# Performance work log

Hardware: AMD Instinct MI355X
Metric: run time of the kernel (lower is better)

The kernel has to match this reference:

```python
import jax, jax.numpy as jnp
import numpy as np

# Model dims (match init_kwargs)
E = 16            # real experts
Z = 16            # zero experts (identity)
TOP_K = 4
H = 1024          # hidden_size
I = 512           # intermediate_size per expert
T = 4096          # tokens
ROUTED_SCALING = 1.0


def setup_inputs() -> dict:
    key = jax.random.key(0)
    ks = jax.random.split(key, 6)
    s_h = 1.0 / np.sqrt(H)
    s_i = 1.0 / np.sqrt(I)
    return {
        "hidden_states": jax.random.normal(ks[0], (T, H), jnp.float32),
        # router over E + Z total slots (real experts + zero experts)
        "router_weight": jax.random.normal(ks[1], (E + Z, H), jnp.float32) * s_h,
        "e_score_bias": jax.random.normal(ks[2], (E + Z,), jnp.float32) * 0.01,
        # SwiGLU expert weights
        "w_gate": jax.random.normal(ks[3], (E, H, I), jnp.float32) * s_h,
        "w_up": jax.random.normal(ks[4], (E, H, I), jnp.float32) * s_h,
        "w_down": jax.random.normal(ks[5], (E, I, H), jnp.float32) * s_i,
    }


def reference(hidden_states, router_weight, e_score_bias, w_gate, w_up, w_down):
    x = hidden_states  # [T, H]
    # --- Router (float32, router_dtype == 'float32') ---
    logits = jnp.einsum("th,eh->te", x.astype(jnp.float32), router_weight)  # [T, E+Z]
    scores = jax.nn.softmax(logits, axis=-1)
    # top-k selected on bias-corrected scores; weights taken from raw scores,
    # renormalize=False
    _, topk_ids = jax.lax.top_k(scores + e_score_bias[None, :], TOP_K)  # [T, k]
    topk_w = jnp.take_along_axis(scores, topk_ids, axis=-1)             # [T, k]
    # --- Dispatch/combine weights over all E+Z slots ---
    onehot = jax.nn.one_hot(topk_ids, E + Z, dtype=jnp.float32)  # [T, k, E+Z]
    combine = jnp.einsum("tk,tks->ts", topk_w, onehot)           # [T, E+Z]
    cw_real = combine[:, :E].astype(x.dtype)      # [T, E] routed-expert weights
    zero_w = combine[:, E:].sum(-1).astype(x.dtype)  # [T] identity weight sum
    # --- Grouped-expert SwiGLU (dense dispatch reference) ---
    g = jnp.einsum("th,ehi->eti", x, w_gate)   # [E, T, I]
    u = jnp.einsum("th,ehi->eti", x, w_up)     # [E, T, I]
    act = jax.nn.silu(g) * u
    eout = jnp.einsum("eti,eih->eth", act, w_down)  # [E, T, H]
    routed = jnp.einsum("eth,te->th", eout, cw_real)  # [T, H]
    # zero experts: identity contribution (zero_expert_type == 'identity')
    out = routed * ROUTED_SCALING + zero_w[:, None] * x
    return out
```

## Files before the change

kernel.cpp:

```cpp
#include <hip/hip_runtime.h>
#include <stdint.h>

#define T_TOK 4096
#define Hd    1024
#define Id    512
#define NE    16
#define NSLOT 32
#define TOPK  4
#define ECAP  1024
#define MAXT  (NE * (ECAP/128))

typedef __bf16 bf16x8 __attribute__((ext_vector_type(8)));
typedef float  floatx4 __attribute__((ext_vector_type(4)));

#define WAIT_VM(n) asm volatile("s_waitcnt vmcnt(" #n ")" ::: "memory")

static __device__ __forceinline__ void wg_barrier(){
  asm volatile("" ::: "memory");
  __builtin_amdgcn_s_barrier();
  asm volatile("" ::: "memory");
}

static __device__ __forceinline__ unsigned short f2bf(float f){
  unsigned int u = __float_as_uint(f);
  u = u + 0x7fffu + ((u >> 16) & 1u);
  return (unsigned short)(u >> 16);
}

static __device__ __forceinline__ void load_lds16(const void* g, void* l){
  __builtin_amdgcn_global_load_lds((const __attribute__((address_space(1))) void*)g,
                                   (__attribute__((address_space(3))) void*)l, 16, 0, 0);
}

__global__ __launch_bounds__(256) void prep_kernel(
    const float* __restrict__ wg, const float* __restrict__ wu,
    const float* __restrict__ wd, const float* __restrict__ x,
    const float* __restrict__ rw,
    unsigned short* __restrict__ wgb, unsigned short* __restrict__ wub,
    unsigned short* __restrict__ wdb, unsigned short* __restrict__ xb,
    float* __restrict__ logits, int* __restrict__ cursors){
  __shared__ float shbuf[2*64*65];
  const int bid = blockIdx.x;
  const int tid = threadIdx.x;
  if (bid < 640){
    const float* src; unsigned short* dst; int R, C, e, r0;
    if (bid < 256)      { src = wg; dst = wgb; R = Hd; C = Id; e = bid >> 4;        r0 = (bid & 15) * 64; }
    else if (bid < 512) { src = wu; dst = wub; R = Hd; C = Id; e = (bid - 256) >> 4; r0 = (bid & 15) * 64; }
    else                { src = wd; dst = wdb; R = Id; C = Hd; e = (bid - 512) >> 3; r0 = ((bid - 512) & 7) * 64; }
    const int J = C >> 6;
    const float* s = src + (size_t)e * R * C + (size_t)r0 * C;
    unsigned short* d = dst + (size_t)e * R * C + r0;
    const int lr = tid >> 4;
    const int lc = (tid & 15) * 4;
    float* b0 = shbuf;
    float* b1 = shbuf + 64*65;
    float4 v[4];
    #pragma unroll
    for (int p = 0; p < 4; ++p)
      v[p] = *(const float4*)(s + (size_t)(p*16 + lr)*C + lc);
    #pragma unroll
    for (int p = 0; p < 4; ++p){
      float* row = b0 + (p*16 + lr)*65 + lc;
      row[0] = v[p].x; row[1] = v[p].y; row[2] = v[p].z; row[3] = v[p].w;
    }
    __syncthreads();
    for (int j = 0; j < J; ++j){
      float* cur = (j & 1) ? b1 : b0;
      float* nxt = (j & 1) ? b0 : b1;
      if (j + 1 < J){
        const int c0n = (j + 1) * 64;
        #pragma unroll
        for (int p = 0; p < 4; ++p)
          v[p] = *(const float4*)(s + (size_t)(p*16 + lr)*C + c0n + lc);
      }
      const int c0 = j * 64;
      #pragma unroll
      for (int p = 0; p < 4; ++p){
        int c = p*16 + lr;
        ushort4 o;
        o.x = f2bf(cur[(lc+0)*65 + c]); o.y = f2bf(cur[(lc+1)*65 + c]);
        o.z = f2bf(cur[(lc+2)*65 + c]); o.w = f2bf(cur[(lc+3)*65 + c]);
        *(ushort4*)(d + (size_t)(c0 + c)*R + lc) = o;
      }
      if (j + 1 < J){
        #pragma unroll
        for (int p = 0; p < 4; ++p){
          float* row = nxt + (p*16 + lr)*65 + lc;
          row[0] = v[p].x; row[1] = v[p].y; row[2] = v[p].z; row[3] = v[p].w;
        }
      }
      __syncthreads();
    }
  } else if (bid < 1664){
    const int ib = (bid - 640) * 1024;
    #pragma unroll
    for (int p = 0; p < 4; ++p){
      int i = ib + p*256 + tid;
      float4 v = ((const float4*)x)[i];
      ushort4 o;
      o.x = f2bf(v.x); o.y = f2bf(v.y); o.z = f2bf(v.z); o.w = f2bf(v.w);
      ((ushort4*)xb)[i] = o;
    }
  } else {
    const int lb = bid - 1664;
    if (lb == 0 && tid < NE) cursors[tid] = 0;
    float* srw = shbuf;
    const int t  = lb * 32 + (tid >> 3);
    const int s0 = tid & 7;
    float4 acc = {0.f, 0.f, 0.f, 0.f};
    for (int c = 0; c < 4; ++c){
      const int kc = c * 256;
      __syncthreads();
      #pragma unroll
      for (int p = 0; p < 8; ++p){
        int idx = tid + p*256;
        int s = idx >> 6;
        int col = (idx & 63) << 2;
        *(float4*)&srw[s*260 + col] = *(const float4*)(rw + (size_t)s*Hd + kc + col);
      }
      __syncthreads();
      for (int k = 0; k < 256; k += 4){
        float4 xv = *(const float4*)(x + (size_t)t*Hd + kc + k);
        float4 r0 = *(const float4*)&srw[(s0+ 0)*260 + k];
        float4 r1 = *(const float4*)&srw[(s0+ 8)*260 + k];
        float4 r2 = *(const float4*)&srw[(s0+16)*260 + k];
        float4 r3 = *(const float4*)&srw[(s0+24)*260 + k];
        acc.x += xv.x*r0.x + xv.y*r0.y + xv.z*r0.z + xv.w*r0.w;
        acc.y += xv.x*r1.x + xv.y*r1.y + xv.z*r1.z + xv.w*r1.w;
        acc.z += xv.x*r2.x + xv.y*r2.y + xv.z*r2.z + xv.w*r2.w;
        acc.w += xv.x*r3.x + xv.y*r3.y + xv.z*r3.z + xv.w*r3.w;
      }
    }
    logits[(size_t)t*NSLOT + s0     ] = acc.x;
    logits[(size_t)t*NSLOT + s0 +  8] = acc.y;
    logits[(size_t)t*NSLOT + s0 + 16] = acc.z;
    logits[(size_t)t*NSLOT + s0 + 24] = acc.w;
  }
}

__global__ __launch_bounds__(256) void topk_kernel(
    const float* __restrict__ logits, const float* __restrict__ bias,
    const float* __restrict__ x,
    int* __restrict__ cursors, int* __restrict__ rowmap, float* __restrict__ roww,
    float* __restrict__ out){
  __shared__ float szw[8];
  const int tid = threadIdx.x;
  if (tid < 8){
    const int t = blockIdx.x * 8 + tid;
    float sc[32], bsc[32];
    #pragma unroll
    for (int i = 0; i < 32; i += 4){
      float4 v = *(const float4*)(logits + (size_t)t*NSLOT + i);
      sc[i] = v.x; sc[i+1] = v.y; sc[i+2] = v.z; sc[i+3] = v.w;
    }
    float mx = sc[0];
    #pragma unroll
    for (int i = 1; i < 32; ++i) mx = fmaxf(mx, sc[i]);
    float sum = 0.f;
    #pragma unroll
    for (int i = 0; i < 32; ++i){ sc[i] = __expf(sc[i]-mx); sum += sc[i]; }
    float inv = 1.f / sum;
    #pragma unroll
    for (int i = 0; i < 32; ++i){ sc[i] *= inv; bsc[i] = sc[i] + bias[i]; }
    unsigned int chosen = 0;
    float zw = 0.f;
    #pragma unroll
    for (int k = 0; k < TOPK; ++k){
      float bv = -1e30f, bw = 0.f; int best = 0;
      #pragma unroll
      for (int i = 0; i < 32; ++i){
        float v = ((chosen >> i) & 1u) ? -1e30f : bsc[i];
        if (v > bv){ bv = v; best = i; bw = sc[i]; }
      }
      chosen |= (1u << best);
      if (best < NE){
        int pos = atomicAdd(&cursors[best], 1);
        rowmap[best*ECAP + pos] = t;
        roww[best*ECAP + pos]   = bw;
      } else zw += bw;
    }
    szw[tid] = zw;
  }
  __syncthreads();
  const int lane = tid & 63, wid = tid >> 6;
  const size_t base = (size_t)blockIdx.x * 8 * Hd;
  #pragma unroll
  for (int r0 = 0; r0 < 8; r0 += 4){
    int r = r0 + wid;
    float s = szw[r];
    const float4* xs = (const float4*)(x + base + (size_t)r*Hd);
    float4* os = (float4*)(out + base + (size_t)r*Hd);
    #pragma unroll
    for (int q = 0; q < 4; ++q){
      float4 v = xs[lane + q*64];
      float4 o; o.x = v.x*s; o.y = v.y*s; o.z = v.z*s; o.w = v.w*s;
      os[lane + q*64] = o;
    }
  }
}

static __device__ __forceinline__ bool tile_map(const int* __restrict__ counts, int tile,
                                                int& e, int& off, int& ne, int& m0){
  int cumT = 0; e = -1; ne = 0; m0 = 0;
  #pragma unroll
  for (int ee = 0; ee < NE; ++ee){
    int c = counts[ee];
    int nt = (c + 127) >> 7;
    bool here = (e < 0) && (tile < cumT + nt);
    if (here){ e = ee; ne = c; m0 = (tile - cumT) * 128; }
    cumT += nt;
  }
  off = (e >= 0) ? e * ECAP : 0;
  return e >= 0;
}

__global__ __launch_bounds__(256, 2) void gateup_kernel(
    const unsigned short* __restrict__ xb,
    const unsigned short* __restrict__ wgb,
    const unsigned short* __restrict__ wub,
    const int* __restrict__ counts,
    const int* __restrict__ rowmap,
    const float* __restrict__ roww,
    unsigned short* __restrict__ act){
  const int b = blockIdx.x;
  int e, off, ne, m0;
  if (!tile_map(counts, b >> 2, e, off, ne, m0)) return;
  const int n0 = (b & 3) * 128;

  __shared__ unsigned short sA [2][128*32];
  __shared__ unsigned short sBg[2][128*32];
  __shared__ unsigned short sBu[2][128*32];
  __shared__ int sT[128];

  const int tid  = threadIdx.x;
  const int lane = tid & 63;
  const int wid  = tid >> 6;

  if (tid < 128){
    int r = m0 + tid;
    sT[tid] = rowmap[off + ((r < ne) ? r : 0)];
  }
  __syncthreads();

  const int r_in = lane >> 2;
  const int seg  = lane & 3;
  const int rt0  = wid*32 + r_in;
  const int rt1  = rt0 + 16;
  const size_t wbase = (size_t)e * Id * Hd;

  const unsigned short* pA0 = xb + (size_t)sT[rt0]*Hd + seg*8;
  const unsigned short* pA1 = xb + (size_t)sT[rt1]*Hd + seg*8;
  const unsigned short* pG0 = wgb + wbase + (size_t)(n0+rt0)*Hd + seg*8;
  const unsigned short* pG1 = wgb + wbase + (size_t)(n0+rt1)*Hd + seg*8;
  const unsigned short* pU0 = wub + wbase + (size_t)(n0+rt0)*Hd + seg*8;
  const unsigned short* pU1 = wub + wbase + (size_t)(n0+rt1)*Hd + seg*8;
  const int dA0 = wid*1024;
  const int dA1 = wid*1024 + 512;

  floatx4 accg[4][4], accu[4][4];
  #pragma unroll
  for (int i = 0; i < 4; ++i)
    #pragma unroll
    for (int j = 0; j < 4; ++j){
      floatx4 z = {0.f,0.f,0.f,0.f};
      accg[i][j] = z; accu[i][j] = z;
    }

  const int wm = (wid & 1) * 64;
  const int wn = (wid >> 1) * 64;
  const int fm = lane & 15;
  const int fq = lane >> 4;

  load_lds16(pA0, &sA[0][dA0]);  load_lds16(pA1, &sA[0][dA1]);
  load_lds16(pG0, &sBg[0][dA0]); load_lds16(pG1, &sBg[0][dA1]);
  load_lds16(pU0, &sBu[0][dA0]); load_lds16(pU1, &sBu[0][dA1]);

  #pragma unroll 2
  for (int kit = 0; kit < 32; ++kit){
    const int cur = kit & 1;
    if (kit < 31){
      const int nk = (kit+1)*32;
      const int nb = 1 - cur;
      load_lds16(pA0 + nk, &sA[nb][dA0]);  load_lds16(pA1 + nk, &sA[nb][dA1]);
      load_lds16(pG0 + nk, &sBg[nb][dA0]); load_lds16(pG1 + nk, &sBg[nb][dA1]);
      load_lds16(pU0 + nk, &sBu[nb][dA0]); load_lds16(pU1 + nk, &sBu[nb][dA1]);
      WAIT_VM(6);
    } else {
      WAIT_VM(0);
    }
    wg_barrier();
    bf16x8 av[4], bgv[4], buv[4];
    #pragma unroll
    for (int i = 0; i < 4; ++i)
      av[i] = *(const bf16x8*)(&sA[cur][(wm + i*16 + fm)*32 + fq*8]);
    #pragma unroll
    for (int j = 0; j < 4; ++j){
      bgv[j] = *(const bf16x8*)(&sBg[cur][(wn + j*16 + fm)*32 + fq*8]);
      buv[j] = *(const bf16x8*)(&sBu[cur][(wn + j*16 + fm)*32 + fq*8]);
    }
    #pragma unroll
    for (int i = 0; i < 4; ++i)
      #pragma unroll
      for (int j = 0; j < 4; ++j){
        accg[i][j] = __builtin_amdgcn_mfma_f32_16x16x32_bf16(av[i], bgv[j], accg[i][j], 0, 0, 0);
        accu[i][j] = __builtin_amdgcn_mfma_f32_16x16x32_bf16(av[i], buv[j], accu[i][j], 0, 0, 0);
      }
    wg_barrier();
  }

  #pragma unroll
  for (int i = 0; i < 4; ++i){
    #pragma unroll
    for (int r = 0; r < 4; ++r){
      int row = wm + i*16 + fq*4 + r;
      if (m0 + row < ne){
        float w = roww[off + m0 + row];
        size_t rb = (size_t)(off + m0 + row) * Id + n0;
        #pragma unroll
        for (int j = 0; j < 4; ++j){
          float g = accg[i][j][r];
          float u = accu[i][j][r];
          float a = (g / (1.f + __expf(-g))) * u * w;
          act[rb + wn + j*16 + fm] = f2bf(a);
        }
      }
    }
  }
}

__global__ __launch_bounds__(256, 4) void down_kernel(
    const unsigned short* __restrict__ act,
    const unsigned short* __restrict__ wdb,
    const int* __restrict__ counts,
    const int* __restrict__ rowmap,
    float* __restrict__ out){
  const int b = blockIdx.x;
  int e, off, ne, m0;
  if (!tile_map(counts, b >> 3, e, off, ne, m0)) return;
  const int n0 = (b & 7) * 128;

  __shared__ unsigned short sA[2][128*32];
  __shared__ unsigned short sB[2][128*32];
  __shared__ int sT[128];

  const int tid  = threadIdx.x;
  const int lane = tid & 63;
  const int wid  = tid >> 6;
  if (tid < 128){
    int r = m0 + tid;
    sT[tid] = (r < ne) ? rowmap[off + r] : 0;
  }

  const int r_in = lane >> 2, seg = lane & 3;
  const int rt0 = wid*32 + r_in;
  const int rt1 = rt0 + 16;
  const int gr0 = off + ((m0 + rt0 < ne) ? (m0 + rt0) : 0);
  const int gr1 = off + ((m0 + rt1 < ne) ? (m0 + rt1) : 0);
  const size_t wbase = (size_t)e * Hd * Id;
  const unsigned short* pA0 = act + (size_t)gr0*Id + seg*8;
  const unsigned short* pA1 = act + (size_t)gr1*Id + seg*8;
  const unsigned short* pB0 = wdb + wbase + (size_t)(n0+rt0)*Id + seg*8;
  const unsigned short* pB1 = wdb + wbase + (size_t)(n0+rt1)*Id + seg*8;
  const int dA0 = wid*1024, dA1 = wid*1024 + 512;

  floatx4 acc[4][4];
  #pragma unroll
  for (int i = 0; i < 4; ++i)
    #pragma unroll
    for (int j = 0; j < 4; ++j){ floatx4 z = {0.f,0.f,0.f,0.f}; acc[i][j] = z; }

  const int wm = (wid & 1) * 64, wn = (wid >> 1) * 64;
  const int fm = lane & 15, fq = lane >> 4;

  load_lds16(pA0, &sA[0][dA0]); load_lds16(pA1, &sA[0][dA1]);
  load_lds16(pB0, &sB[0][dA0]); load_lds16(pB1, &sB[0][dA1]);

  #pragma unroll 2
  for (int kit = 0; kit < 16; ++kit){
    const int cur = kit & 1;
    if (kit < 15){
      const int nk = (kit+1)*32;
      const int nb = 1 - cur;
      load_lds16(pA0 + nk, &sA[nb][dA0]); load_lds16(pA1 + nk, &sA[nb][dA1]);
      load_lds16(pB0 + nk, &sB[nb][dA0]); load_lds16(pB1 + nk, &sB[nb][dA1]);
      WAIT_VM(4);
    } else {
      WAIT_VM(0);
    }
    wg_barrier();
    bf16x8 av[4], bv[4];
    #pragma unroll
    for (int i = 0; i < 4; ++i) av[i] = *(const bf16x8*)(&sA[cur][(wm + i*16 + fm)*32 + fq*8]);
    #pragma unroll
    for (int j = 0; j < 4; ++j) bv[j] = *(const bf16x8*)(&sB[cur][(wn + j*16 + fm)*32 + fq*8]);
    #pragma unroll
    for (int i = 0; i < 4; ++i)
      #pragma unroll
      for (int j = 0; j < 4; ++j)
        acc[i][j] = __builtin_amdgcn_mfma_f32_16x16x32_bf16(av[i], bv[j], acc[i][j], 0, 0, 0);
    wg_barrier();
  }

  #pragma unroll
  for (int i = 0; i < 4; ++i){
    #pragma unroll
    for (int r = 0; r < 4; ++r){
      int row = wm + i*16 + fq*4 + r;
      if (m0 + row < ne){
        int t = sT[row];
        #pragma unroll
        for (int j = 0; j < 4; ++j)
          atomicAdd(&out[(size_t)t*Hd + n0 + wn + j*16 + fm], acc[i][j][r]);
      }
    }
  }
}

extern "C" void kernel_launch(void* const* d_in, const int* in_sizes, int n_in,
                              void* d_out, int out_size, void* d_ws, size_t ws_size,
                              hipStream_t stream){
  (void)in_sizes; (void)n_in; (void)out_size; (void)ws_size;
  const float* x    = (const float*)d_in[0];
  const float* rw   = (const float*)d_in[1];
  const float* bias = (const float*)d_in[2];
  const float* wg   = (const float*)d_in[3];
  const float* wu   = (const float*)d_in[4];
  const float* wd   = (const float*)d_in[5];
  float* out = (float*)d_out;

  char* ws = (char*)d_ws;
  const size_t WSZ = (size_t)NE * Id * Hd * 2;
  unsigned short* wgb = (unsigned short*)(ws);
  unsigned short* wub = (unsigned short*)(ws + WSZ);
  unsigned short* wdb = (unsigned short*)(ws + 2*WSZ);
  unsigned short* xb  = (unsigned short*)(ws + 3*WSZ);
  unsigned short* act = (unsigned short*)(ws + 3*WSZ + (size_t)T_TOK*Hd*2);
  char* misc = ws + 3*WSZ + (size_t)T_TOK*Hd*2 + (size_t)NE*ECAP*Id*2;

  const size_t LOGB = (size_t)T_TOK * NSLOT * 4;
  float* logits  = (float*)misc;
  int*   cursors = (int*)(misc + LOGB);
  char* p2 = misc + LOGB + 256;
  int*   rowmap = (int*)p2;                     p2 += (size_t)NE*ECAP*4;
  float* roww   = (float*)p2;

  prep_kernel<<<1792, 256, 0, stream>>>(wg, wu, wd, x, rw,
                                        wgb, wub, wdb, xb, logits, cursors);
  topk_kernel<<<T_TOK/8, 256, 0, stream>>>(logits, bias, x, cursors, rowmap, roww, out);
  gateup_kernel<<<MAXT*4, 256, 0, stream>>>(xb, wgb, wub, cursors, rowmap, roww, act);
  down_kernel<<<MAXT*8, 256, 0, stream>>>(act, wdb, cursors, rowmap, out);
}
```

Measured before the change: 304.4 us.

## Fuse fp32-to-bf16 weight conversion into the expert GEMM B-tile loads

Drops the separate prep pass that transposed and converted all expert weights to bf16. The gate/up and down GEMMs now read fp32 weights directly into registers, truncate pairs to bf16 with a byte permute, and write them into padded LDS tiles, with a register prefetch two iterations ahead. This removes a full read and write of the weight tensors per call, at the cost of reading fp32 weights once per token tile and spending VALU time on packing. Weight rounding changes from round-to-nearest to truncation, and the barrier is replaced with explicit lgkmcnt waits.

```diff
diff --git a/kernel.cpp b/kernel.cpp
--- a/kernel.cpp
+++ b/kernel.cpp
@@ -14,11 +14,13 @@
 typedef float  floatx4 __attribute__((ext_vector_type(4)));
 
 #define WAIT_VM(n) asm volatile("s_waitcnt vmcnt(" #n ")" ::: "memory")
-
+#define CFENCE()   asm volatile("" ::: "memory")
+
+static __device__ __forceinline__ void barrier_lgkm(){
+  asm volatile("s_waitcnt lgkmcnt(0)\ns_barrier" ::: "memory");
+}
 static __device__ __forceinline__ void wg_barrier(){
-  asm volatile("" ::: "memory");
-  __builtin_amdgcn_s_barrier();
-  asm volatile("" ::: "memory");
+  asm volatile("s_barrier" ::: "memory");
 }
 
 static __device__ __forceinline__ unsigned short f2bf(float f){
@@ -32,69 +34,39 @@
                                    (__attribute__((address_space(3))) void*)l, 16, 0, 0);
 }
 
+struct B8 { float4 a0, a1, b0, b1; };
+
+static __device__ __forceinline__ B8 loadB(const float* p, int S){
+  B8 r;
+  r.a0 = *(const float4*)(p);
+  r.a1 = *(const float4*)(p + 4);
+  r.b0 = *(const float4*)(p + S);
+  r.b1 = *(const float4*)(p + S + 4);
+  return r;
+}
+
+static __device__ __forceinline__ void packB(const B8& r, uint32_t* dst, int ng8, int kq){
+  dst[(ng8+0)*20 + kq] = __builtin_amdgcn_perm(__float_as_uint(r.b0.x), __float_as_uint(r.a0.x), 0x07060302u);
+  dst[(ng8+1)*20 + kq] = __builtin_amdgcn_perm(__float_as_uint(r.b0.y), __float_as_uint(r.a0.y), 0x07060302u);
+  dst[(ng8+2)*20 + kq] = __builtin_amdgcn_perm(__float_as_uint(r.b0.z), __float_as_uint(r.a0.z), 0x07060302u);
+  dst[(ng8+3)*20 + kq] = __builtin_amdgcn_perm(__float_as_uint(r.b0.w), __float_as_uint(r.a0.w), 0x07060302u);
+  dst[(ng8+4)*20 + kq] = __builtin_amdgcn_perm(__float_as_uint(r.b1.x), __float_as_uint(r.a1.x), 0x07060302u);
+  dst[(ng8+5)*20 + kq] = __builtin_amdgcn_perm(__float_as_uint(r.b1.y), __float_as_uint(r.a1.y), 0x07060302u);
+  dst[(ng8+6)*20 + kq] = __builtin_amdgcn_perm(__float_as_uint(r.b1.z), __float_as_uint(r.a1.z), 0x07060302u);
+  dst[(ng8+7)*20 + kq] = __builtin_amdgcn_perm(__float_as_uint(r.b1.w), __float_as_uint(r.a1.w), 0x07060302u);
+}
+
 __global__ __launch_bounds__(256) void prep_kernel(
-    const float* __restrict__ wg, const float* __restrict__ wu,
-    const float* __restrict__ wd, const float* __restrict__ x,
-    const float* __restrict__ rw,
-    unsigned short* __restrict__ wgb, unsigned short* __restrict__ wub,
-    unsigned short* __restrict__ wdb, unsigned short* __restrict__ xb,
-    float* __restrict__ logits, int* __restrict__ cursors){
-  __shared__ float shbuf[2*64*65];
+    const float* __restrict__ x, const float* __restrict__ rw,
+    unsigned short* __restrict__ xb, float* __restrict__ logits,
+    int* __restrict__ cursors){
+  __shared__ float srw[NSLOT*260];
   const int bid = blockIdx.x;
   const int tid = threadIdx.x;
-  if (bid < 640){
-    const float* src; unsigned short* dst; int R, C, e, r0;
-    if (bid < 256)      { src = wg; dst = wgb; R = Hd; C = Id; e = bid >> 4;        r0 = (bid & 15) * 64; }
-    else if (bid < 512) { src = wu; dst = wub; R = Hd; C = Id; e = (bid - 256) >> 4; r0 = (bid & 15) * 64; }
-    else                { src = wd; dst = wdb; R = Id; C = Hd; e = (bid - 512) >> 3; r0 = ((bid - 512) & 7) * 64; }
-    const int J = C >> 6;
-    const float* s = src + (size_t)e * R * C + (size_t)r0 * C;
-    unsigned short* d = dst + (size_t)e * R * C + r0;
-    const int lr = tid >> 4;
-    const int lc = (tid & 15) * 4;
-    float* b0 = shbuf;
-    float* b1 = shbuf + 64*65;
-    float4 v[4];
-    #pragma unroll
-    for (int p = 0; p < 4; ++p)
-      v[p] = *(const float4*)(s + (size_t)(p*16 + lr)*C + lc);
-    #pragma unroll
-    for (int p = 0; p < 4; ++p){
-      float* row = b0 + (p*16 + lr)*65 + lc;
-      row[0] = v[p].x; row[1] = v[p].y; row[2] = v[p].z; row[3] = v[p].w;
-    }
-    __syncthreads();
-    for (int j = 0; j < J; ++j){
-      float* cur = (j & 1) ? b1 : b0;
-      float* nxt = (j & 1) ? b0 : b1;
-      if (j + 1 < J){
-        const int c0n = (j + 1) * 64;
-        #pragma unroll
-        for (int p = 0; p < 4; ++p)
-          v[p] = *(const float4*)(s + (size_t)(p*16 + lr)*C + c0n + lc);
-      }
-      const int c0 = j * 64;
-      #pragma unroll
-      for (int p = 0; p < 4; ++p){
-        int c = p*16 + lr;
-        ushort4 o;
-        o.x = f2bf(cur[(lc+0)*65 + c]); o.y = f2bf(cur[(lc+1)*65 + c]);
-        o.z = f2bf(cur[(lc+2)*65 + c]); o.w = f2bf(cur[(lc+3)*65 + c]);
-        *(ushort4*)(d + (size_t)(c0 + c)*R + lc) = o;
-      }
-      if (j + 1 < J){
-        #pragma unroll
-        for (int p = 0; p < 4; ++p){
-          float* row = nxt + (p*16 + lr)*65 + lc;
-          row[0] = v[p].x; row[1] = v[p].y; row[2] = v[p].z; row[3] = v[p].w;
-        }
-      }
-      __syncthreads();
-    }
-  } else if (bid < 1664){
-    const int ib = (bid - 640) * 1024;
-    #pragma unroll
-    for (int p = 0; p < 4; ++p){
+  if (bid < 256){
+    const int ib = bid * 4096;
+    #pragma unroll
+    for (int p = 0; p < 16; ++p){
       int i = ib + p*256 + tid;
       float4 v = ((const float4*)x)[i];
       ushort4 o;
@@ -102,9 +74,8 @@
       ((ushort4*)xb)[i] = o;
     }
   } else {
-    const int lb = bid - 1664;
+    const int lb = bid - 256;
     if (lb == 0 && tid < NE) cursors[tid] = 0;
-    float* srw = shbuf;
     const int t  = lb * 32 + (tid >> 3);
     const int s0 = tid & 7;
     float4 acc = {0.f, 0.f, 0.f, 0.f};
@@ -216,46 +187,34 @@
 
 __global__ __launch_bounds__(256, 2) void gateup_kernel(
     const unsigned short* __restrict__ xb,
-    const unsigned short* __restrict__ wgb,
-    const unsigned short* __restrict__ wub,
-    const int* __restrict__ counts,
-    const int* __restrict__ rowmap,
-    const float* __restrict__ roww,
-    unsigned short* __restrict__ act){
+    const float* __restrict__ wg, const float* __restrict__ wu,
+    const int* __restrict__ counts, const int* __restrict__ rowmap,
+    const float* __restrict__ roww, unsigned short* __restrict__ act){
   const int b = blockIdx.x;
   int e, off, ne, m0;
   if (!tile_map(counts, b >> 2, e, off, ne, m0)) return;
   const int n0 = (b & 3) * 128;
 
   __shared__ unsigned short sA [2][128*32];
-  __shared__ unsigned short sBg[2][128*32];
-  __shared__ unsigned short sBu[2][128*32];
+  __shared__ unsigned short sBg[2][128*40];
+  __shared__ unsigned short sBu[2][128*40];
   __shared__ int sT[128];
 
-  const int tid  = threadIdx.x;
-  const int lane = tid & 63;
-  const int wid  = tid >> 6;
-
-  if (tid < 128){
-    int r = m0 + tid;
-    sT[tid] = rowmap[off + ((r < ne) ? r : 0)];
-  }
+  const int tid = threadIdx.x, lane = tid & 63, wid = tid >> 6;
+  if (tid < 128){ int r = m0 + tid; sT[tid] = rowmap[off + ((r < ne) ? r : 0)]; }
   __syncthreads();
 
-  const int r_in = lane >> 2;
-  const int seg  = lane & 3;
-  const int rt0  = wid*32 + r_in;
-  const int rt1  = rt0 + 16;
-  const size_t wbase = (size_t)e * Id * Hd;
-
+  const int r_in = lane >> 2, seg = lane & 3;
+  const int rt0 = wid*32 + r_in, rt1 = rt0 + 16;
   const unsigned short* pA0 = xb + (size_t)sT[rt0]*Hd + seg*8;
   const unsigned short* pA1 = xb + (size_t)sT[rt1]*Hd + seg*8;
-  const unsigned short* pG0 = wgb + wbase + (size_t)(n0+rt0)*Hd + seg*8;
-  const unsigned short* pG1 = wgb + wbase + (size_t)(n0+rt1)*Hd + seg*8;
-  const unsigned short* pU0 = wub + wbase + (size_t)(n0+rt0)*Hd + seg*8;
-  const unsigned short* pU1 = wub + wbase + (size_t)(n0+rt1)*Hd + seg*8;
-  const int dA0 = wid*1024;
-  const int dA1 = wid*1024 + 512;
+  const int dA0 = wid*1024, dA1 = wid*1024 + 512;
+
+  const size_t wbase = (size_t)e * Hd * Id;
+  const int ng8 = (tid >> 4) * 8;
+  const int kq  = tid & 15;
+  const float* pG = wg + wbase + (size_t)(kq*2)*Id + n0 + ng8;
+  const float* pU = wu + wbase + (size_t)(kq*2)*Id + n0 + ng8;
 
   floatx4 accg[4][4], accu[4][4];
   #pragma unroll
@@ -265,38 +224,44 @@
       floatx4 z = {0.f,0.f,0.f,0.f};
       accg[i][j] = z; accu[i][j] = z;
     }
-
-  const int wm = (wid & 1) * 64;
-  const int wn = (wid >> 1) * 64;
-  const int fm = lane & 15;
-  const int fq = lane >> 4;
-
-  load_lds16(pA0, &sA[0][dA0]);  load_lds16(pA1, &sA[0][dA1]);
-  load_lds16(pG0, &sBg[0][dA0]); load_lds16(pG1, &sBg[0][dA1]);
-  load_lds16(pU0, &sBu[0][dA0]); load_lds16(pU1, &sBu[0][dA1]);
-
-  #pragma unroll 2
+  const int wm = (wid & 1) * 64, wn = (wid >> 1) * 64;
+  const int fm = lane & 15, fq = lane >> 4;
+
+  B8 rg = loadB(pG, Id);
+  B8 ru = loadB(pU, Id);
+  load_lds16(pA0, &sA[0][dA0]); load_lds16(pA1, &sA[0][dA1]);
+  CFENCE();
+  packB(rg, (uint32_t*)&sBg[0][0], ng8, kq);
+  packB(ru, (uint32_t*)&sBu[0][0], ng8, kq);
+  CFENCE();
+  rg = loadB(pG + (size_t)32*Id, Id);
+  ru = loadB(pU + (size_t)32*Id, Id);
+
   for (int kit = 0; kit < 32; ++kit){
     const int cur = kit & 1;
     if (kit < 31){
-      const int nk = (kit+1)*32;
       const int nb = 1 - cur;
-      load_lds16(pA0 + nk, &sA[nb][dA0]);  load_lds16(pA1 + nk, &sA[nb][dA1]);
-      load_lds16(pG0 + nk, &sBg[nb][dA0]); load_lds16(pG1 + nk, &sBg[nb][dA1]);
-      load_lds16(pU0 + nk, &sBu[nb][dA0]); load_lds16(pU1 + nk, &sBu[nb][dA1]);
-      WAIT_VM(6);
-    } else {
-      WAIT_VM(0);
-    }
-    wg_barrier();
+      const int nk = (kit + 1) * 32;
+      load_lds16(pA0 + nk, &sA[nb][dA0]);
+      load_lds16(pA1 + nk, &sA[nb][dA1]);
+      CFENCE();
+      packB(rg, (uint32_t*)&sBg[nb][0], ng8, kq);
+      packB(ru, (uint32_t*)&sBu[nb][0], ng8, kq);
+      CFENCE();
+      const size_t k2 = (size_t)((kit < 30) ? (kit + 2) : 31) * 32;
+      rg = loadB(pG + k2*Id, Id);
+      ru = loadB(pU + k2*Id, Id);
+      WAIT_VM(8);
+    }
+    barrier_lgkm();
     bf16x8 av[4], bgv[4], buv[4];
     #pragma unroll
     for (int i = 0; i < 4; ++i)
       av[i] = *(const bf16x8*)(&sA[cur][(wm + i*16 + fm)*32 + fq*8]);
     #pragma unroll
     for (int j = 0; j < 4; ++j){
-      bgv[j] = *(const bf16x8*)(&sBg[cur][(wn + j*16 + fm)*32 + fq*8]);
-      buv[j] = *(const bf16x8*)(&sBu[cur][(wn + j*16 + fm)*32 + fq*8]);
+      bgv[j] = *(const bf16x8*)(&sBg[cur][(wn + j*16 + fm)*40 + fq*8]);
+      buv[j] = *(const bf16x8*)(&sBu[cur][(wn + j*16 + fm)*40 + fq*8]);
     }
     #pragma unroll
     for (int i = 0; i < 4; ++i)
@@ -330,9 +295,8 @@
 
 __global__ __launch_bounds__(256, 4) void down_kernel(
     const unsigned short* __restrict__ act,
-    const unsigned short* __restrict__ wdb,
-    const int* __restrict__ counts,
-    const int* __restrict__ rowmap,
+    const float* __restrict__ wd,
+    const int* __restrict__ counts, const int* __restrict__ rowmap,
     float* __restrict__ out){
   const int b = blockIdx.x;
   int e, off, ne, m0;
@@ -340,59 +304,61 @@
   const int n0 = (b & 7) * 128;
 
   __shared__ unsigned short sA[2][128*32];
-  __shared__ unsigned short sB[2][128*32];
+  __shared__ unsigned short sB[2][128*40];
   __shared__ int sT[128];
 
-  const int tid  = threadIdx.x;
-  const int lane = tid & 63;
-  const int wid  = tid >> 6;
-  if (tid < 128){
-    int r = m0 + tid;
-    sT[tid] = (r < ne) ? rowmap[off + r] : 0;
-  }
+  const int tid = threadIdx.x, lane = tid & 63, wid = tid >> 6;
+  if (tid < 128){ int r = m0 + tid; sT[tid] = (r < ne) ? rowmap[off + r] : 0; }
+  __syncthreads();
 
   const int r_in = lane >> 2, seg = lane & 3;
-  const int rt0 = wid*32 + r_in;
-  const int rt1 = rt0 + 16;
+  const int rt0 = wid*32 + r_in, rt1 = rt0 + 16;
   const int gr0 = off + ((m0 + rt0 < ne) ? (m0 + rt0) : 0);
   const int gr1 = off + ((m0 + rt1 < ne) ? (m0 + rt1) : 0);
-  const size_t wbase = (size_t)e * Hd * Id;
   const unsigned short* pA0 = act + (size_t)gr0*Id + seg*8;
   const unsigned short* pA1 = act + (size_t)gr1*Id + seg*8;
-  const unsigned short* pB0 = wdb + wbase + (size_t)(n0+rt0)*Id + seg*8;
-  const unsigned short* pB1 = wdb + wbase + (size_t)(n0+rt1)*Id + seg*8;
   const int dA0 = wid*1024, dA1 = wid*1024 + 512;
 
+  const size_t wbase = (size_t)e * Id * Hd;
+  const int ng8 = (tid >> 4) * 8;
+  const int kq  = tid & 15;
+  const float* pB = wd + wbase + (size_t)(kq*2)*Hd + n0 + ng8;
+
   floatx4 acc[4][4];
   #pragma unroll
   for (int i = 0; i < 4; ++i)
     #pragma unroll
     for (int j = 0; j < 4; ++j){ floatx4 z = {0.f,0.f,0.f,0.f}; acc[i][j] = z; }
-
   const int wm = (wid & 1) * 64, wn = (wid >> 1) * 64;
   const int fm = lane & 15, fq = lane >> 4;
 
+  B8 rb = loadB(pB, Hd);
   load_lds16(pA0, &sA[0][dA0]); load_lds16(pA1, &sA[0][dA1]);
-  load_lds16(pB0, &sB[0][dA0]); load_lds16(pB1, &sB[0][dA1]);
-
-  #pragma unroll 2
+  CFENCE();
+  packB(rb, (uint32_t*)&sB[0][0], ng8, kq);
+  CFENCE();
+  rb = loadB(pB + (size_t)32*Hd, Hd);
+
   for (int kit = 0; kit < 16; ++kit){
     const int cur = kit & 1;
     if (kit < 15){
-      const int nk = (kit+1)*32;
       const int nb = 1 - cur;
-      load_lds16(pA0 + nk, &sA[nb][dA0]); load_lds16(pA1 + nk, &sA[nb][dA1]);
-      load_lds16(pB0 + nk, &sB[nb][dA0]); load_lds16(pB1 + nk, &sB[nb][dA1]);
+      const int nk = (kit + 1) * 32;
+      load_lds16(pA0 + nk, &sA[nb][dA0]);
+      load_lds16(pA1 + nk, &sA[nb][dA1]);
+      CFENCE();
+      packB(rb, (uint32_t*)&sB[nb][0], ng8, kq);
+      CFENCE();
+      const size_t k2 = (size_t)((kit < 14) ? (kit + 2) : 15) * 32;
+      rb = loadB(pB + k2*Hd, Hd);
       WAIT_VM(4);
-    } else {
-      WAIT_VM(0);
-    }
-    wg_barrier();
+    }
+    barrier_lgkm();
     bf16x8 av[4], bv[4];
     #pragma unroll
     for (int i = 0; i < 4; ++i) av[i] = *(const bf16x8*)(&sA[cur][(wm + i*16 + fm)*32 + fq*8]);
     #pragma unroll
-    for (int j = 0; j < 4; ++j) bv[j] = *(const bf16x8*)(&sB[cur][(wn + j*16 + fm)*32 + fq*8]);
+    for (int j = 0; j < 4; ++j) bv[j] = *(const bf16x8*)(&sB[cur][(wn + j*16 + fm)*40 + fq*8]);
     #pragma unroll
     for (int i = 0; i < 4; ++i)
       #pragma unroll
@@ -429,13 +395,9 @@
   float* out = (float*)d_out;
 
   char* ws = (char*)d_ws;
-  const size_t WSZ = (size_t)NE * Id * Hd * 2;
-  unsigned short* wgb = (unsigned short*)(ws);
-  unsigned short* wub = (unsigned short*)(ws + WSZ);
-  unsigned short* wdb = (unsigned short*)(ws + 2*WSZ);
-  unsigned short* xb  = (unsigned short*)(ws + 3*WSZ);
-  unsigned short* act = (unsigned short*)(ws + 3*WSZ + (size_t)T_TOK*Hd*2);
-  char* misc = ws + 3*WSZ + (size_t)T_TOK*Hd*2 + (size_t)NE*ECAP*Id*2;
+  unsigned short* xb  = (unsigned short*)ws;
+  unsigned short* act = (unsigned short*)(ws + (size_t)T_TOK*Hd*2);
+  char* misc = ws + (size_t)T_TOK*Hd*2 + (size_t)NE*ECAP*Id*2;
 
   const size_t LOGB = (size_t)T_TOK * NSLOT * 4;
   float* logits  = (float*)misc;
@@ -444,9 +406,8 @@
   int*   rowmap = (int*)p2;                     p2 += (size_t)NE*ECAP*4;
   float* roww   = (float*)p2;
 
-  prep_kernel<<<1792, 256, 0, stream>>>(wg, wu, wd, x, rw,
-                                        wgb, wub, wdb, xb, logits, cursors);
+  prep_kernel<<<384, 256, 0, stream>>>(x, rw, xb, logits, cursors);
   topk_kernel<<<T_TOK/8, 256, 0, stream>>>(logits, bias, x, cursors, rowmap, roww, out);
-  gateup_kernel<<<MAXT*4, 256, 0, stream>>>(xb, wgb, wub, cursors, rowmap, roww, act);
-  down_kernel<<<MAXT*8, 256, 0, stream>>>(act, wdb, cursors, rowmap, out);
-}
+  gateup_kernel<<<MAXT*4, 256, 0, stream>>>(xb, wg, wu, cursors, rowmap, roww, act);
+  down_kernel<<<MAXT*8, 256, 0, stream>>>(act, wd, cursors, rowmap, out);
+}
```

Result: slower. 312.6 us (+2.7%).

## Restructure prep kernel: register-only weight transpose, reordered router and x-convert blocks

Applied to the files above, without the earlier changes.

Rewrites the weight fp32→bf16 transpose so each block handles one 64x64 tile held entirely in registers. Each thread loads four rows of float4 and packs the bf16 pairs with a byte permute, which truncates instead of rounding. This removes the LDS staging, the barriers and the serial per-row loop, and spreads the work across many more blocks. The router-logit blocks now come first with 16 threads per token, and the x conversion uses fewer, larger blocks. In exchange, the transposed stores are 8-byte strided writes rather than coalesced ones, and the truncating conversion changes numerics slightly.

```diff
diff --git a/kernel.cpp b/kernel.cpp
--- a/kernel.cpp
+++ b/kernel.cpp
@@ -27,6 +27,10 @@
   return (unsigned short)(u >> 16);
 }
 
+static __device__ __forceinline__ uint32_t bfpack(uint32_t hi_src, uint32_t lo_src){
+  return __builtin_amdgcn_perm(hi_src, lo_src, 0x07060302u);
+}
+
 static __device__ __forceinline__ void load_lds16(const void* g, void* l){
   __builtin_amdgcn_global_load_lds((const __attribute__((address_space(1))) void*)g,
                                    (__attribute__((address_space(3))) void*)l, 16, 0, 0);
@@ -39,75 +43,14 @@
     unsigned short* __restrict__ wgb, unsigned short* __restrict__ wub,
     unsigned short* __restrict__ wdb, unsigned short* __restrict__ xb,
     float* __restrict__ logits, int* __restrict__ cursors){
-  __shared__ float shbuf[2*64*65];
   const int bid = blockIdx.x;
   const int tid = threadIdx.x;
-  if (bid < 640){
-    const float* src; unsigned short* dst; int R, C, e, r0;
-    if (bid < 256)      { src = wg; dst = wgb; R = Hd; C = Id; e = bid >> 4;        r0 = (bid & 15) * 64; }
-    else if (bid < 512) { src = wu; dst = wub; R = Hd; C = Id; e = (bid - 256) >> 4; r0 = (bid & 15) * 64; }
-    else                { src = wd; dst = wdb; R = Id; C = Hd; e = (bid - 512) >> 3; r0 = ((bid - 512) & 7) * 64; }
-    const int J = C >> 6;
-    const float* s = src + (size_t)e * R * C + (size_t)r0 * C;
-    unsigned short* d = dst + (size_t)e * R * C + r0;
-    const int lr = tid >> 4;
-    const int lc = (tid & 15) * 4;
-    float* b0 = shbuf;
-    float* b1 = shbuf + 64*65;
-    float4 v[4];
-    #pragma unroll
-    for (int p = 0; p < 4; ++p)
-      v[p] = *(const float4*)(s + (size_t)(p*16 + lr)*C + lc);
-    #pragma unroll
-    for (int p = 0; p < 4; ++p){
-      float* row = b0 + (p*16 + lr)*65 + lc;
-      row[0] = v[p].x; row[1] = v[p].y; row[2] = v[p].z; row[3] = v[p].w;
-    }
-    __syncthreads();
-    for (int j = 0; j < J; ++j){
-      float* cur = (j & 1) ? b1 : b0;
-      float* nxt = (j & 1) ? b0 : b1;
-      if (j + 1 < J){
-        const int c0n = (j + 1) * 64;
-        #pragma unroll
-        for (int p = 0; p < 4; ++p)
-          v[p] = *(const float4*)(s + (size_t)(p*16 + lr)*C + c0n + lc);
-      }
-      const int c0 = j * 64;
-      #pragma unroll
-      for (int p = 0; p < 4; ++p){
-        int c = p*16 + lr;
-        ushort4 o;
-        o.x = f2bf(cur[(lc+0)*65 + c]); o.y = f2bf(cur[(lc+1)*65 + c]);
-        o.z = f2bf(cur[(lc+2)*65 + c]); o.w = f2bf(cur[(lc+3)*65 + c]);
-        *(ushort4*)(d + (size_t)(c0 + c)*R + lc) = o;
-      }
-      if (j + 1 < J){
-        #pragma unroll
-        for (int p = 0; p < 4; ++p){
-          float* row = nxt + (p*16 + lr)*65 + lc;
-          row[0] = v[p].x; row[1] = v[p].y; row[2] = v[p].z; row[3] = v[p].w;
-        }
-      }
-      __syncthreads();
-    }
-  } else if (bid < 1664){
-    const int ib = (bid - 640) * 1024;
-    #pragma unroll
-    for (int p = 0; p < 4; ++p){
-      int i = ib + p*256 + tid;
-      float4 v = ((const float4*)x)[i];
-      ushort4 o;
-      o.x = f2bf(v.x); o.y = f2bf(v.y); o.z = f2bf(v.z); o.w = f2bf(v.w);
-      ((ushort4*)xb)[i] = o;
-    }
-  } else {
-    const int lb = bid - 1664;
-    if (lb == 0 && tid < NE) cursors[tid] = 0;
-    float* srw = shbuf;
-    const int t  = lb * 32 + (tid >> 3);
-    const int s0 = tid & 7;
-    float4 acc = {0.f, 0.f, 0.f, 0.f};
+  if (bid < 256){
+    __shared__ float srw[NSLOT*260];
+    if (bid == 0 && tid < NE) cursors[tid] = 0;
+    const int t  = bid * 16 + (tid >> 4);
+    const int s0 = tid & 15;
+    float accx = 0.f, accy = 0.f;
     for (int c = 0; c < 4; ++c){
       const int kc = c * 256;
       __syncthreads();
@@ -121,20 +64,54 @@
       __syncthreads();
       for (int k = 0; k < 256; k += 4){
         float4 xv = *(const float4*)(x + (size_t)t*Hd + kc + k);
-        float4 r0 = *(const float4*)&srw[(s0+ 0)*260 + k];
-        float4 r1 = *(const float4*)&srw[(s0+ 8)*260 + k];
-        float4 r2 = *(const float4*)&srw[(s0+16)*260 + k];
-        float4 r3 = *(const float4*)&srw[(s0+24)*260 + k];
-        acc.x += xv.x*r0.x + xv.y*r0.y + xv.z*r0.z + xv.w*r0.w;
-        acc.y += xv.x*r1.x + xv.y*r1.y + xv.z*r1.z + xv.w*r1.w;
-        acc.z += xv.x*r2.x + xv.y*r2.y + xv.z*r2.z + xv.w*r2.w;
-        acc.w += xv.x*r3.x + xv.y*r3.y + xv.z*r3.z + xv.w*r3.w;
-      }
-    }
-    logits[(size_t)t*NSLOT + s0     ] = acc.x;
-    logits[(size_t)t*NSLOT + s0 +  8] = acc.y;
-    logits[(size_t)t*NSLOT + s0 + 16] = acc.z;
-    logits[(size_t)t*NSLOT + s0 + 24] = acc.w;
+        float4 r0 = *(const float4*)&srw[(s0     )*260 + k];
+        float4 r1 = *(const float4*)&srw[(s0 + 16)*260 + k];
+        accx += xv.x*r0.x + xv.y*r0.y + xv.z*r0.z + xv.w*r0.w;
+        accy += xv.x*r1.x + xv.y*r1.y + xv.z*r1.z + xv.w*r1.w;
+      }
+    }
+    logits[(size_t)t*NSLOT + s0     ] = accx;
+    logits[(size_t)t*NSLOT + s0 + 16] = accy;
+  } else if (bid < 512){
+    const int ib = (bid - 256) * 4096;
+    #pragma unroll
+    for (int p = 0; p < 16; ++p){
+      int i = ib + p*256 + tid;
+      float4 v = ((const float4*)x)[i];
+      ushort4 o;
+      o.x = f2bf(v.x); o.y = f2bf(v.y); o.z = f2bf(v.z); o.w = f2bf(v.w);
+      ((ushort4*)xb)[i] = o;
+    }
+  } else {
+    const int tb = bid - 512;
+    const float* src; unsigned short* dst; int R, C, rt, ct;
+    const int arr = tb >> 11;
+    const int rem = tb & 2047;
+    const int e  = rem >> 7;
+    const int t2 = rem & 127;
+    if (arr == 0)      { src = wg; dst = wgb; R = Hd; C = Id; rt = t2 >> 3; ct = t2 & 7;  }
+    else if (arr == 1) { src = wu; dst = wub; R = Hd; C = Id; rt = t2 >> 3; ct = t2 & 7;  }
+    else               { src = wd; dst = wdb; R = Id; C = Hd; rt = t2 >> 4; ct = t2 & 15; }
+    const int r0 = rt * 64, c0 = ct * 64;
+    const float* s = src + (size_t)e * R * C;
+    unsigned short* d = dst + (size_t)e * R * C;
+    const int r_idx = tid >> 4;
+    const int c_idx = tid & 15;
+    const int rr = r0 + r_idx * 4;
+    const int cc = c0 + c_idx * 4;
+    uint4 u0 = *(const uint4*)(s + (size_t)(rr + 0)*C + cc);
+    uint4 u1 = *(const uint4*)(s + (size_t)(rr + 1)*C + cc);
+    uint4 u2 = *(const uint4*)(s + (size_t)(rr + 2)*C + cc);
+    uint4 u3 = *(const uint4*)(s + (size_t)(rr + 3)*C + cc);
+    uint2 o;
+    o.x = bfpack(u1.x, u0.x); o.y = bfpack(u3.x, u2.x);
+    *(uint2*)(d + (size_t)(cc + 0)*R + rr) = o;
+    o.x = bfpack(u1.y, u0.y); o.y = bfpack(u3.y, u2.y);
+    *(uint2*)(d + (size_t)(cc + 1)*R + rr) = o;
+    o.x = bfpack(u1.z, u0.z); o.y = bfpack(u3.z, u2.z);
+    *(uint2*)(d + (size_t)(cc + 2)*R + rr) = o;
+    o.x = bfpack(u1.w, u0.w); o.y = bfpack(u3.w, u2.w);
+    *(uint2*)(d + (size_t)(cc + 3)*R + rr) = o;
   }
 }
 
@@ -232,20 +209,12 @@
   __shared__ unsigned short sBu[2][128*32];
   __shared__ int sT[128];
 
-  const int tid  = threadIdx.x;
-  const int lane = tid & 63;
-  const int wid  = tid >> 6;
-
-  if (tid < 128){
-    int r = m0 + tid;
-    sT[tid] = rowmap[off + ((r < ne) ? r : 0)];
-  }
+  const int tid = threadIdx.x, lane = tid & 63, wid = tid >> 6;
+  if (tid < 128){ int r = m0 + tid; sT[tid] = rowmap[off + ((r < ne) ? r : 0)]; }
   __syncthreads();
 
-  const int r_in = lane >> 2;
-  const int seg  = lane & 3;
-  const int rt0  = wid*32 + r_in;
-  const int rt1  = rt0 + 16;
+  const int r_in = lane >> 2, seg = lane & 3;
+  const int rt0 = wid*32 + r_in, rt1 = rt0 + 16;
   const size_t wbase = (size_t)e * Id * Hd;
 
   const unsigned short* pA0 = xb + (size_t)sT[rt0]*Hd + seg*8;
@@ -254,8 +223,7 @@
   const unsigned short* pG1 = wgb + wbase + (size_t)(n0+rt1)*Hd + seg*8;
   const unsigned short* pU0 = wub + wbase + (size_t)(n0+rt0)*Hd + seg*8;
   const unsigned short* pU1 = wub + wbase + (size_t)(n0+rt1)*Hd + seg*8;
-  const int dA0 = wid*1024;
-  const int dA1 = wid*1024 + 512;
+  const int dA0 = wid*1024, dA1 = wid*1024 + 512;
 
   floatx4 accg[4][4], accu[4][4];
   #pragma unroll
@@ -265,11 +233,8 @@
       floatx4 z = {0.f,0.f,0.f,0.f};
       accg[i][j] = z; accu[i][j] = z;
     }
-
-  const int wm = (wid & 1) * 64;
-  const int wn = (wid >> 1) * 64;
-  const int fm = lane & 15;
-  const int fq = lane >> 4;
+  const int wm = (wid & 1) * 64, wn = (wid >> 1) * 64;
+  const int fm = lane & 15, fq = lane >> 4;
 
   load_lds16(pA0, &sA[0][dA0]);  load_lds16(pA1, &sA[0][dA1]);
   load_lds16(pG0, &sBg[0][dA0]); load_lds16(pG1, &sBg[0][dA1]);
@@ -343,17 +308,11 @@
   __shared__ unsigned short sB[2][128*32];
   __shared__ int sT[128];
 
-  const int tid  = threadIdx.x;
-  const int lane = tid & 63;
-  const int wid  = tid >> 6;
-  if (tid < 128){
-    int r = m0 + tid;
-    sT[tid] = (r < ne) ? rowmap[off + r] : 0;
-  }
+  const int tid = threadIdx.x, lane = tid & 63, wid = tid >> 6;
+  if (tid < 128){ int r = m0 + tid; sT[tid] = (r < ne) ? rowmap[off + r] : 0; }
 
   const int r_in = lane >> 2, seg = lane & 3;
-  const int rt0 = wid*32 + r_in;
-  const int rt1 = rt0 + 16;
+  const int rt0 = wid*32 + r_in, rt1 = rt0 + 16;
   const int gr0 = off + ((m0 + rt0 < ne) ? (m0 + rt0) : 0);
   const int gr1 = off + ((m0 + rt1 < ne) ? (m0 + rt1) : 0);
   const size_t wbase = (size_t)e * Hd * Id;
@@ -368,7 +327,6 @@
   for (int i = 0; i < 4; ++i)
     #pragma unroll
     for (int j = 0; j < 4; ++j){ floatx4 z = {0.f,0.f,0.f,0.f}; acc[i][j] = z; }
-
   const int wm = (wid & 1) * 64, wn = (wid >> 1) * 64;
   const int fm = lane & 15, fq = lane >> 4;
 
@@ -444,7 +402,7 @@
   int*   rowmap = (int*)p2;                     p2 += (size_t)NE*ECAP*4;
   float* roww   = (float*)p2;
 
-  prep_kernel<<<1792, 256, 0, stream>>>(wg, wu, wd, x, rw,
+  prep_kernel<<<6656, 256, 0, stream>>>(wg, wu, wd, x, rw,
                                         wgb, wub, wdb, xb, logits, cursors);
   topk_kernel<<<T_TOK/8, 256, 0, stream>>>(logits, bias, x, cursors, rowmap, roww, out);
   gateup_kernel<<<MAXT*4, 256, 0, stream>>>(xb, wgb, wub, cursors, rowmap, roww, act);
```

Result: faster. 284.4 us (-6.5%).
